# Kernel optimization log

Measured on AMD Instinct MI355X. Metric: run time of the kernel, lower is better.

Reference implementation:

```python
import jax, jax.numpy as jnp
import numpy as np

B, S, D, H = 2, 2048, 1024, 16
DK = D // H


def setup_inputs() -> dict:
    key = jax.random.key(0)
    ks = jax.random.split(key, 8)
    Q = jax.random.normal(ks[0], (B, S, D), dtype=jnp.float32)
    K = jax.random.normal(ks[1], (B, S, D), dtype=jnp.float32)
    V = jax.random.normal(ks[2], (B, S, D), dtype=jnp.float32)
    # causal mask (1 = keep), broadcastable to [B, H, S, S]
    mask = jnp.tril(jnp.ones((S, S), dtype=bool))[None, None, :, :]
    # xavier_uniform for [D, D]: bound = sqrt(6 / (D + D))
    bound = float(np.sqrt(6.0 / (D + D)))
    def xavier(k):
        return jax.random.uniform(k, (D, D), jnp.float32, -bound, bound)
    Wq, Wk, Wv, Wo = xavier(ks[3]), xavier(ks[4]), xavier(ks[5]), xavier(ks[6])
    bq = jnp.zeros((D,), jnp.float32)
    bk = jnp.zeros((D,), jnp.float32)
    bv = jnp.zeros((D,), jnp.float32)
    bo = jnp.zeros((D,), jnp.float32)
    return {"Q": Q, "K": K, "V": V, "mask": mask,
            "Wq": Wq, "bq": bq, "Wk": Wk, "bk": bk,
            "Wv": Wv, "bv": bv, "Wo": Wo, "bo": bo}


def _split_heads(x):
    # [B, S, D] -> [B, H, S, DK]
    b, s, _ = x.shape
    return x.reshape(b, s, H, DK).transpose(0, 2, 1, 3)


def reference(Q, K, V, mask, Wq, bq, Wk, bk, Wv, bv, Wo, bo):
    # linear projections (torch Linear: x @ W.T + b)
    q = _split_heads(Q @ Wq.T + bq)  # [B, H, S, DK]
    k = _split_heads(K @ Wk.T + bk)
    v = _split_heads(V @ Wv.T + bv)
    scale = 1.0 / jnp.sqrt(jnp.asarray(DK, q.dtype))
    scores = jnp.einsum('bhqd,bhkd->bhqk', q, k) * scale  # [B, H, S, S]
    scores = jnp.where(mask, scores, jnp.asarray(-1e9, scores.dtype))
    attn = jax.nn.softmax(scores, axis=-1)
    ctx = jnp.einsum('bhqk,bhkd->bhqd', attn, v)  # [B, H, S, DK]
    ctx = ctx.transpose(0, 2, 1, 3).reshape(Q.shape[0], Q.shape[1], D)
    out = ctx @ Wo.T + bo  # dropout is identity in eval mode
    return out, attn
```

## Files before the change

### kernel.cpp

```cpp
#include <hip/hip_runtime.h>
#include <hip/hip_bf16.h>

#define B_  2
#define S_  2048
#define D_  1024
#define H_  16
#define DK_ 64
#define M_  (B_*S_)
#define NT_ (S_/64)
#define NE_ (B_*S_*D_)
#define NW_ (D_*D_)

typedef __attribute__((ext_vector_type(8))) short short8;
typedef __attribute__((ext_vector_type(4))) float f32x4;

static __device__ __forceinline__ unsigned short f2bf(float f) {
    union { float f; unsigned u; } v; v.f = f;
    unsigned r = (v.u + 0x7fffu + ((v.u >> 16) & 1u)) >> 16;
    return (unsigned short)r;
}

static __device__ __forceinline__ void gload16(const void* g, void* l) {
    __builtin_amdgcn_global_load_lds((const __attribute__((address_space(1))) void*)g,
                                     (__attribute__((address_space(3))) void*)l, 16, 0, 0);
}

__global__ __launch_bounds__(256) void conv7(const float* __restrict__ q,  const float* __restrict__ k,
                                             const float* __restrict__ v,  const float* __restrict__ wq,
                                             const float* __restrict__ wk, const float* __restrict__ wv,
                                             const float* __restrict__ wo, unsigned short* __restrict__ ws)
{
    const float* src[7] = {q, k, v, wq, wk, wv, wo};
    const int    n4[7]  = {NE_/4, NE_/4, NE_/4, NW_/4, NW_/4, NW_/4, NW_/4};
    size_t off = 0;
    #pragma unroll
    for (int seg = 0; seg < 7; ++seg) {
        unsigned short* dst = ws + off;
        for (int i = blockIdx.x*256 + threadIdx.x; i < n4[seg]; i += gridDim.x*256) {
            float4 x = ((const float4*)src[seg])[i];
            union { unsigned short u[4]; unsigned long long ll; } cv;
            cv.u[0]=f2bf(x.x); cv.u[1]=f2bf(x.y); cv.u[2]=f2bf(x.z); cv.u[3]=f2bf(x.w);
            ((unsigned long long*)dst)[i] = cv.ll;
        }
        off += (size_t)n4[seg]*4;
    }
}

__global__ __launch_bounds__(256) void gemm_bt(const unsigned short* __restrict__ A0,
                                               const unsigned short* __restrict__ W0,
                                               const float* __restrict__ b0,
                                               const float* __restrict__ b1,
                                               const float* __restrict__ b2,
                                               void* __restrict__ outv,
                                               void* __restrict__ outv2,
                                               int out_mode)
{
    __shared__ unsigned short as_[128][64];
    __shared__ unsigned short bs_[128][64];

    const int tid  = threadIdx.x;
    const int wave = tid >> 6;
    const int lane = tid & 63;
    const int lq   = lane & 15, quad = lane >> 4;

    const int g     = blockIdx.x;
    const int xcd   = g & 7;
    const int local = g >> 3;
    const int m_loc = local & 3;
    const int rest  = local >> 2;
    const int n_t   = rest & 7;
    const int z     = rest >> 3;

    const int m0 = (xcd*4 + m_loc) * 128;
    const int n0 = n_t * 128;
    const int wm = (wave >> 1) * 64, wn = (wave & 1) * 64;

    const unsigned short* A  = A0 + (size_t)z * NE_;
    const unsigned short* Bt = W0 + (size_t)z * NW_;
    const float* bias = (z == 0) ? b0 : (z == 1 ? b1 : b2);

    f32x4 acc[4][4] = {};

    for (int k0 = 0; k0 < D_; k0 += 64) {
        __syncthreads();
        #pragma unroll
        for (int i = 0; i < 4; ++i) {
            const int p = tid + i*256, row = p >> 3, c = (p & 7) ^ (row & 7);
            gload16(A + (size_t)(m0+row)*D_ + k0 + c*8,
                    (char*)as_ + (size_t)(wave*64 + i*256)*16);
        }
        #pragma unroll
        for (int i = 0; i < 4; ++i) {
            const int p = tid + i*256, row = p >> 3, c = (p & 7) ^ (row & 7);
            gload16(Bt + (size_t)(n0+row)*D_ + k0 + c*8,
                    (char*)bs_ + (size_t)(wave*64 + i*256)*16);
        }
        __syncthreads();

        #pragma unroll
        for (int kk = 0; kk < 2; ++kk) {
            short8 a[4], b[4];
            #pragma unroll
            for (int i = 0; i < 4; ++i) {
                const int row = wm + i*16 + lq;
                a[i] = *(const short8*)((const char*)as_ + row*128 + (((kk*4+quad) ^ (row&7))*16));
            }
            #pragma unroll
            for (int j = 0; j < 4; ++j) {
                const int row = wn + j*16 + lq;
                b[j] = *(const short8*)((const char*)bs_ + row*128 + (((kk*4+quad) ^ (row&7))*16));
            }
            #pragma unroll
            for (int i = 0; i < 4; ++i)
                #pragma unroll
                for (int j = 0; j < 4; ++j)
                    acc[i][j] = __builtin_amdgcn_mfma_f32_16x16x32_bf16(a[i], b[j], acc[i][j], 0, 0, 0);
        }
    }

    float bcol[4];
    #pragma unroll
    for (int j = 0; j < 4; ++j) bcol[j] = bias[n0 + wn + j*16 + lq];

    if (out_mode == 0) {
        float* out = (float*)outv;
        #pragma unroll
        for (int i = 0; i < 4; ++i)
            #pragma unroll
            for (int j = 0; j < 4; ++j) {
                const int col = n0 + wn + j*16 + lq;
                #pragma unroll
                for (int r = 0; r < 4; ++r) {
                    const int m = m0 + wm + i*16 + quad*4 + r;
                    out[(size_t)m*D_ + col] = acc[i][j][r] + bcol[j];
                }
            }
    } else if (z < 2) {
        unsigned short* out = (unsigned short*)outv + (size_t)z * NE_;
        #pragma unroll
        for (int i = 0; i < 4; ++i)
            #pragma unroll
            for (int j = 0; j < 4; ++j) {
                const int col = n0 + wn + j*16 + lq;
                const int h = col >> 6, dk = col & 63;
                #pragma unroll
                for (int r = 0; r < 4; ++r) {
                    const int m  = m0 + wm + i*16 + quad*4 + r;
                    const int bb = m >> 11, s = m & (S_-1);
                    out[(((size_t)(bb*H_ + h))*S_ + s)*DK_ + dk] = f2bf(acc[i][j][r] + bcol[j]);
                }
            }
    } else {
        unsigned short* out = (unsigned short*)outv2;
        #pragma unroll
        for (int i = 0; i < 4; ++i)
            #pragma unroll
            for (int j = 0; j < 4; ++j) {
                const int col = n0 + wn + j*16 + lq;
                const int h = col >> 6, dk = col & 63;
                const int m  = m0 + wm + i*16 + quad*4;
                const int bb = m >> 11, s = m & (S_-1);
                union { unsigned short u[4]; unsigned long long ll; } pk;
                #pragma unroll
                for (int r = 0; r < 4; ++r) pk.u[r] = f2bf(acc[i][j][r] + bcol[j]);
                *(unsigned long long*)&out[(((size_t)(bb*H_ + h))*DK_ + dk)*S_ + s] = pk.ll;
            }
    }
}

__global__ __launch_bounds__(256) void attn_mfma(const unsigned short* __restrict__ q,
                                                 const unsigned short* __restrict__ k,
                                                 const unsigned short* __restrict__ vt,
                                                 float* __restrict__ attn,
                                                 unsigned short* __restrict__ ctx)
{
    __shared__ unsigned short qs[2][64][64];
    __shared__ unsigned short ks[64][64];
    __shared__ unsigned short vts[64][64];
    __shared__ unsigned short es[4][16][72];

    const int tid  = threadIdx.x;
    const int wave = tid >> 6, lane = tid & 63;
    const int lq   = lane & 15, quad = lane >> 4;

    const int g = blockIdx.x;
    const int xcd = g & 7, i5 = g >> 3;
    const int x = i5 >> 2;
    const int bhid = xcd + 8*(i5 & 3);
    const int h = bhid & (H_-1), b = bhid >> 4;

    const int itA = x, itB = NT_-1 - x;
    const size_t bh = (size_t)(b*H_ + h);
    const unsigned short* kb  = k  + bh*S_*DK_;
    const unsigned short* vtb = vt + bh*(size_t)DK_*S_;
    const unsigned short* qbA = q + (bh*S_ + (size_t)itA*64) * DK_;
    const unsigned short* qbB = q + (bh*S_ + (size_t)itB*64) * DK_;
    float* attn_bA = attn + bh*(size_t)S_*S_ + (size_t)itA*64*S_;
    float* attn_bB = attn + bh*(size_t)S_*S_ + (size_t)itB*64*S_;

    #pragma unroll
    for (int t = 0; t < 2; ++t) {
        const unsigned short* qb = t ? qbB : qbA;
        #pragma unroll
        for (int i = 0; i < 2; ++i) {
            const int p = tid + i*256, row = p >> 3, c = (p & 7) ^ (row & 7);
            gload16(qb + (size_t)row*DK_ + c*8,
                    (char*)&qs[t][0][0] + (size_t)(wave*64 + i*256)*16);
        }
    }
    __syncthreads();

    const int wr0  = wave*16;
    const int rgA0 = itA*64 + wr0 + quad*4;
    const int rgB0 = itB*64 + wr0 + quad*4;

    short8 aA0, aA1, aB0, aB1;
    {
        const int row = wr0 + lq;
        const int s0 = ((quad)     ^ (row & 7)) * 16;
        const int s1 = ((4 + quad) ^ (row & 7)) * 16;
        aA0 = *(const short8*)((const char*)&qs[0][row][0] + s0);
        aA1 = *(const short8*)((const char*)&qs[0][row][0] + s1);
        aB0 = *(const short8*)((const char*)&qs[1][row][0] + s0);
        aB1 = *(const short8*)((const char*)&qs[1][row][0] + s1);
    }

    float rsA[4] = {0.f,0.f,0.f,0.f}, rsB[4] = {0.f,0.f,0.f,0.f};
    for (int jt = 0; jt <= itB; ++jt) {
        __syncthreads();
        #pragma unroll
        for (int i = 0; i < 2; ++i) {
            const int p = tid + i*256, row = p >> 3, c = (p & 7) ^ (row & 7);
            gload16(kb + ((size_t)jt*64 + row)*DK_ + c*8,
                    (char*)&ks[0][0] + (size_t)(wave*64 + i*256)*16);
        }
        __syncthreads();
        const int actA = (jt <= itA);
        #pragma unroll
        for (int j = 0; j < 4; ++j) {
            const int krow = j*16 + lq;
            const int s0 = ((quad)     ^ (krow & 7)) * 16;
            const int s1 = ((4 + quad) ^ (krow & 7)) * 16;
            const short8 b0 = *(const short8*)((const char*)&ks[krow][0] + s0);
            const short8 b1 = *(const short8*)((const char*)&ks[krow][0] + s1);
            const int cg = jt*64 + j*16 + lq;
            {
                f32x4 s = {};
                s = __builtin_amdgcn_mfma_f32_16x16x32_bf16(aB0, b0, s, 0, 0, 0);
                s = __builtin_amdgcn_mfma_f32_16x16x32_bf16(aB1, b1, s, 0, 0, 0);
                #pragma unroll
                for (int r = 0; r < 4; ++r)
                    if (cg <= rgB0 + r) rsB[r] += __expf(s[r]*0.125f);
            }
            if (actA) {
                f32x4 s = {};
                s = __builtin_amdgcn_mfma_f32_16x16x32_bf16(aA0, b0, s, 0, 0, 0);
                s = __builtin_amdgcn_mfma_f32_16x16x32_bf16(aA1, b1, s, 0, 0, 0);
                #pragma unroll
                for (int r = 0; r < 4; ++r)
                    if (cg <= rgA0 + r) rsA[r] += __expf(s[r]*0.125f);
            }
        }
    }
    #pragma unroll
    for (int m = 1; m < 16; m <<= 1)
        #pragma unroll
        for (int r = 0; r < 4; ++r) {
            rsA[r] += __shfl_xor(rsA[r], m, 64);
            rsB[r] += __shfl_xor(rsB[r], m, 64);
        }
    float invA[4], invB[4];
    #pragma unroll
    for (int r = 0; r < 4; ++r) { invA[r] = 1.0f/rsA[r]; invB[r] = 1.0f/rsB[r]; }

    f32x4 cA[4] = {}, cB[4] = {};
    for (int jt = 0; jt <= itB; ++jt) {
        __syncthreads();
        #pragma unroll
        for (int i = 0; i < 2; ++i) {
            const int p = tid + i*256, row = p >> 3, c = (p & 7) ^ (row & 7);
            gload16(kb + ((size_t)jt*64 + row)*DK_ + c*8,
                    (char*)&ks[0][0] + (size_t)(wave*64 + i*256)*16);
            gload16(vtb + (size_t)row*S_ + jt*64 + c*8,
                    (char*)&vts[0][0] + (size_t)(wave*64 + i*256)*16);
        }
        __syncthreads();
        const int actA = (jt <= itA);

        #pragma unroll
        for (int j = 0; j < 4; ++j) {
            const int krow = j*16 + lq;
            const int s0 = ((quad)     ^ (krow & 7)) * 16;
            const int s1 = ((4 + quad) ^ (krow & 7)) * 16;
            const short8 b0 = *(const short8*)((const char*)&ks[krow][0] + s0);
            const short8 b1 = *(const short8*)((const char*)&ks[krow][0] + s1);
            const int cg = jt*64 + j*16 + lq;
            f32x4 s = {};
            s = __builtin_amdgcn_mfma_f32_16x16x32_bf16(aB0, b0, s, 0, 0, 0);
            s = __builtin_amdgcn_mfma_f32_16x16x32_bf16(aB1, b1, s, 0, 0, 0);
            #pragma unroll
            for (int r = 0; r < 4; ++r) {
                const float e = (cg <= rgB0 + r) ? __expf(s[r]*0.125f)*invB[r] : 0.f;
                attn_bB[(size_t)(wr0 + quad*4 + r)*S_ + cg] = e;
                es[wave][quad*4 + r][j*16 + lq] = f2bf(e);
            }
        }
        {
            const short8 p0 = *(const short8*)&es[wave][lq][quad*8];
            const short8 p1 = *(const short8*)&es[wave][lq][32 + quad*8];
            #pragma unroll
            for (int j = 0; j < 4; ++j) {
                const int vrow = j*16 + lq;
                const int s0 = ((quad)     ^ (vrow & 7)) * 16;
                const int s1 = ((4 + quad) ^ (vrow & 7)) * 16;
                cB[j] = __builtin_amdgcn_mfma_f32_16x16x32_bf16(
                    p0, *(const short8*)((const char*)&vts[vrow][0] + s0), cB[j], 0, 0, 0);
                cB[j] = __builtin_amdgcn_mfma_f32_16x16x32_bf16(
                    p1, *(const short8*)((const char*)&vts[vrow][0] + s1), cB[j], 0, 0, 0);
            }
        }

        if (actA) {
            #pragma unroll
            for (int j = 0; j < 4; ++j) {
                const int krow = j*16 + lq;
                const int s0 = ((quad)     ^ (krow & 7)) * 16;
                const int s1 = ((4 + quad) ^ (krow & 7)) * 16;
                const short8 b0 = *(const short8*)((const char*)&ks[krow][0] + s0);
                const short8 b1 = *(const short8*)((const char*)&ks[krow][0] + s1);
                const int cg = jt*64 + j*16 + lq;
                f32x4 s = {};
                s = __builtin_amdgcn_mfma_f32_16x16x32_bf16(aA0, b0, s, 0, 0, 0);
                s = __builtin_amdgcn_mfma_f32_16x16x32_bf16(aA1, b1, s, 0, 0, 0);
                #pragma unroll
                for (int r = 0; r < 4; ++r) {
                    const float e = (cg <= rgA0 + r) ? __expf(s[r]*0.125f)*invA[r] : 0.f;
                    attn_bA[(size_t)(wr0 + quad*4 + r)*S_ + cg] = e;
                    es[wave][quad*4 + r][j*16 + lq] = f2bf(e);
                }
            }
            const short8 p0 = *(const short8*)&es[wave][lq][quad*8];
            const short8 p1 = *(const short8*)&es[wave][lq][32 + quad*8];
            #pragma unroll
            for (int j = 0; j < 4; ++j) {
                const int vrow = j*16 + lq;
                const int s0 = ((quad)     ^ (vrow & 7)) * 16;
                const int s1 = ((4 + quad) ^ (vrow & 7)) * 16;
                cA[j] = __builtin_amdgcn_mfma_f32_16x16x32_bf16(
                    p0, *(const short8*)((const char*)&vts[vrow][0] + s0), cA[j], 0, 0, 0);
                cA[j] = __builtin_amdgcn_mfma_f32_16x16x32_bf16(
                    p1, *(const short8*)((const char*)&vts[vrow][0] + s1), cA[j], 0, 0, 0);
            }
        }
    }

    #pragma unroll
    for (int j = 0; j < 4; ++j) {
        const int dk = j*16 + lq;
        #pragma unroll
        for (int r = 0; r < 4; ++r) {
            const int sA = itA*64 + wr0 + quad*4 + r;
            const int sB = itB*64 + wr0 + quad*4 + r;
            ctx[((size_t)b*S_ + sA)*D_ + h*DK_ + dk] = f2bf(cA[j][r]);
            ctx[((size_t)b*S_ + sB)*D_ + h*DK_ + dk] = f2bf(cB[j][r]);
        }
    }

    const float4 z4 = make_float4(0.f, 0.f, 0.f, 0.f);
    {
        const int zc0 = (itA+1)*64;
        float* rowp = attn_bA + (size_t)(tid >> 2)*S_;
        for (int c = zc0 + (tid & 3)*4; c < S_; c += 16) *(float4*)&rowp[c] = z4;
    }
    {
        const int zc0 = (itB+1)*64;
        if (zc0 < S_) {
            float* rowp = attn_bB + (size_t)(tid >> 2)*S_;
            for (int c = zc0 + (tid & 3)*4; c < S_; c += 16) *(float4*)&rowp[c] = z4;
        }
    }
}

extern "C" void kernel_launch(void* const* d_in, const int* in_sizes, int n_in,
                              void* d_out, int out_size, void* d_ws, size_t ws_size,
                              hipStream_t stream)
{
    const float* Q  = (const float*)d_in[0];
    const float* K  = (const float*)d_in[1];
    const float* V  = (const float*)d_in[2];
    const float* Wq = (const float*)d_in[4];
    const float* bq = (const float*)d_in[5];
    const float* Wk = (const float*)d_in[6];
    const float* bk = (const float*)d_in[7];
    const float* Wv = (const float*)d_in[8];
    const float* bv = (const float*)d_in[9];
    const float* Wo = (const float*)d_in[10];
    const float* bo = (const float*)d_in[11];

    float* out  = (float*)d_out;
    float* attn = out + (size_t)B_*S_*D_;

    unsigned short* ws = (unsigned short*)d_ws;
    const size_t R  = (size_t)NE_;
    const size_t W1 = (size_t)NW_;
    unsigned short* Qb  = ws;
    unsigned short* Wqb = ws + 3*R;
    unsigned short* Wob = Wqb + 3*W1;
    unsigned short* qp  = Wob + W1;
    unsigned short* kp  = qp + R;
    unsigned short* vtw = qp + 2*R;
    unsigned short* ctx = vtw + R;

    conv7<<<2048, 256, 0, stream>>>(Q, K, V, Wq, Wk, Wv, Wo, ws);

    gemm_bt<<<768, 256, 0, stream>>>(Qb, Wqb, bq, bk, bv, qp, vtw, 1);
    attn_mfma<<<(NT_/2)*H_*B_, 256, 0, stream>>>(qp, kp, vtw, attn, ctx);
    gemm_bt<<<256, 256, 0, stream>>>(ctx, Wob, bo, bo, bo, out, nullptr, 0);
}
```

Before: 804.2 us.

## Single-pass unnormalized softmax with bf16 scratch and separate normalization kernel

Removes the first pass over K that computed row sums. Each score block is now exponentiated once, unnormalized, with the log2(e)/sqrt(dk) scale folded into the Q projection and a raw v_exp_f32. Unnormalized probabilities go to a bf16 scratch buffer, and the context is scaled by the inverse row sum at the end. A new kernel reads the scratch plus per-row inverse sums and writes the fp32 attention matrix, including the zeroed upper triangle. There is no running max subtraction, so this relies on scores staying small enough not to overflow exp. It also adds an extra bf16 write and read of the full S×S matrix, and the stored attention is rounded through bf16.

```diff
diff --git a/kernel.cpp b/kernel.cpp
--- a/kernel.cpp
+++ b/kernel.cpp
@@ -14,10 +14,20 @@
 typedef __attribute__((ext_vector_type(8))) short short8;
 typedef __attribute__((ext_vector_type(4))) float f32x4;
 
+#define QSCALE 0.18033688011112042f
+
 static __device__ __forceinline__ unsigned short f2bf(float f) {
     union { float f; unsigned u; } v; v.f = f;
     unsigned r = (v.u + 0x7fffu + ((v.u >> 16) & 1u)) >> 16;
     return (unsigned short)r;
+}
+static __device__ __forceinline__ float bf2f(unsigned short u) {
+    union { unsigned u; float f; } v; v.u = (unsigned)u << 16; return v.f;
+}
+static __device__ __forceinline__ float exp2v(float x) {
+    float r;
+    asm("v_exp_f32 %0, %1" : "=v"(r) : "v"(x));
+    return r;
 }
 
 static __device__ __forceinline__ void gload16(const void* g, void* l) {
@@ -136,6 +146,7 @@
                 }
             }
     } else if (z < 2) {
+        const float sc = (z == 0) ? QSCALE : 1.0f;
         unsigned short* out = (unsigned short*)outv + (size_t)z * NE_;
         #pragma unroll
         for (int i = 0; i < 4; ++i)
@@ -147,7 +158,7 @@
                 for (int r = 0; r < 4; ++r) {
                     const int m  = m0 + wm + i*16 + quad*4 + r;
                     const int bb = m >> 11, s = m & (S_-1);
-                    out[(((size_t)(bb*H_ + h))*S_ + s)*DK_ + dk] = f2bf(acc[i][j][r] + bcol[j]);
+                    out[(((size_t)(bb*H_ + h))*S_ + s)*DK_ + dk] = f2bf((acc[i][j][r] + bcol[j]) * sc);
                 }
             }
     } else {
@@ -171,7 +182,8 @@
 __global__ __launch_bounds__(256) void attn_mfma(const unsigned short* __restrict__ q,
                                                  const unsigned short* __restrict__ k,
                                                  const unsigned short* __restrict__ vt,
-                                                 float* __restrict__ attn,
+                                                 unsigned short* __restrict__ eb,
+                                                 float* __restrict__ invb,
                                                  unsigned short* __restrict__ ctx)
 {
     __shared__ unsigned short qs[2][64][64];
@@ -195,8 +207,8 @@
     const unsigned short* vtb = vt + bh*(size_t)DK_*S_;
     const unsigned short* qbA = q + (bh*S_ + (size_t)itA*64) * DK_;
     const unsigned short* qbB = q + (bh*S_ + (size_t)itB*64) * DK_;
-    float* attn_bA = attn + bh*(size_t)S_*S_ + (size_t)itA*64*S_;
-    float* attn_bB = attn + bh*(size_t)S_*S_ + (size_t)itB*64*S_;
+    unsigned short* ebA = eb + (bh*S_ + (size_t)itA*64 + wave*16)*S_;
+    unsigned short* ebB = eb + (bh*S_ + (size_t)itB*64 + wave*16)*S_;
 
     #pragma unroll
     for (int t = 0; t < 2; ++t) {
@@ -226,54 +238,8 @@
     }
 
     float rsA[4] = {0.f,0.f,0.f,0.f}, rsB[4] = {0.f,0.f,0.f,0.f};
-    for (int jt = 0; jt <= itB; ++jt) {
-        __syncthreads();
-        #pragma unroll
-        for (int i = 0; i < 2; ++i) {
-            const int p = tid + i*256, row = p >> 3, c = (p & 7) ^ (row & 7);
-            gload16(kb + ((size_t)jt*64 + row)*DK_ + c*8,
-                    (char*)&ks[0][0] + (size_t)(wave*64 + i*256)*16);
-        }
-        __syncthreads();
-        const int actA = (jt <= itA);
-        #pragma unroll
-        for (int j = 0; j < 4; ++j) {
-            const int krow = j*16 + lq;
-            const int s0 = ((quad)     ^ (krow & 7)) * 16;
-            const int s1 = ((4 + quad) ^ (krow & 7)) * 16;
-            const short8 b0 = *(const short8*)((const char*)&ks[krow][0] + s0);
-            const short8 b1 = *(const short8*)((const char*)&ks[krow][0] + s1);
-            const int cg = jt*64 + j*16 + lq;
-            {
-                f32x4 s = {};
-                s = __builtin_amdgcn_mfma_f32_16x16x32_bf16(aB0, b0, s, 0, 0, 0);
-                s = __builtin_amdgcn_mfma_f32_16x16x32_bf16(aB1, b1, s, 0, 0, 0);
-                #pragma unroll
-                for (int r = 0; r < 4; ++r)
-                    if (cg <= rgB0 + r) rsB[r] += __expf(s[r]*0.125f);
-            }
-            if (actA) {
-                f32x4 s = {};
-                s = __builtin_amdgcn_mfma_f32_16x16x32_bf16(aA0, b0, s, 0, 0, 0);
-                s = __builtin_amdgcn_mfma_f32_16x16x32_bf16(aA1, b1, s, 0, 0, 0);
-                #pragma unroll
-                for (int r = 0; r < 4; ++r)
-                    if (cg <= rgA0 + r) rsA[r] += __expf(s[r]*0.125f);
-            }
-        }
-    }
-    #pragma unroll
-    for (int m = 1; m < 16; m <<= 1)
-        #pragma unroll
-        for (int r = 0; r < 4; ++r) {
-            rsA[r] += __shfl_xor(rsA[r], m, 64);
-            rsB[r] += __shfl_xor(rsB[r], m, 64);
-        }
-    float invA[4], invB[4];
-    #pragma unroll
-    for (int r = 0; r < 4; ++r) { invA[r] = 1.0f/rsA[r]; invB[r] = 1.0f/rsB[r]; }
-
     f32x4 cA[4] = {}, cB[4] = {};
+
     for (int jt = 0; jt <= itB; ++jt) {
         __syncthreads();
         #pragma unroll
@@ -287,25 +253,48 @@
         __syncthreads();
         const int actA = (jt <= itA);
 
-        #pragma unroll
-        for (int j = 0; j < 4; ++j) {
-            const int krow = j*16 + lq;
-            const int s0 = ((quad)     ^ (krow & 7)) * 16;
-            const int s1 = ((4 + quad) ^ (krow & 7)) * 16;
-            const short8 b0 = *(const short8*)((const char*)&ks[krow][0] + s0);
-            const short8 b1 = *(const short8*)((const char*)&ks[krow][0] + s1);
-            const int cg = jt*64 + j*16 + lq;
-            f32x4 s = {};
-            s = __builtin_amdgcn_mfma_f32_16x16x32_bf16(aB0, b0, s, 0, 0, 0);
-            s = __builtin_amdgcn_mfma_f32_16x16x32_bf16(aB1, b1, s, 0, 0, 0);
-            #pragma unroll
-            for (int r = 0; r < 4; ++r) {
-                const float e = (cg <= rgB0 + r) ? __expf(s[r]*0.125f)*invB[r] : 0.f;
-                attn_bB[(size_t)(wr0 + quad*4 + r)*S_ + cg] = e;
-                es[wave][quad*4 + r][j*16 + lq] = f2bf(e);
-            }
-        }
         {
+            f32x4 sa[4];
+            #pragma unroll
+            for (int j = 0; j < 4; ++j) {
+                const int krow = j*16 + lq;
+                const int s0 = ((quad)     ^ (krow & 7)) * 16;
+                const int s1 = ((4 + quad) ^ (krow & 7)) * 16;
+                f32x4 s = {};
+                s = __builtin_amdgcn_mfma_f32_16x16x32_bf16(
+                    aB0, *(const short8*)((const char*)&ks[krow][0] + s0), s, 0, 0, 0);
+                s = __builtin_amdgcn_mfma_f32_16x16x32_bf16(
+                    aB1, *(const short8*)((const char*)&ks[krow][0] + s1), s, 0, 0, 0);
+                sa[j] = s;
+            }
+            if (jt == itB) {
+                #pragma unroll
+                for (int j = 0; j < 4; ++j) {
+                    const int cg = jt*64 + j*16 + lq;
+                    #pragma unroll
+                    for (int r = 0; r < 4; ++r) {
+                        float e = exp2v(sa[j][r]);
+                        if (cg > rgB0 + r) e = 0.f;
+                        rsB[r] += e;
+                        es[wave][quad*4 + r][j*16 + lq] = f2bf(e);
+                    }
+                }
+            } else {
+                #pragma unroll
+                for (int j = 0; j < 4; ++j)
+                    #pragma unroll
+                    for (int r = 0; r < 4; ++r) {
+                        const float e = exp2v(sa[j][r]);
+                        rsB[r] += e;
+                        es[wave][quad*4 + r][j*16 + lq] = f2bf(e);
+                    }
+            }
+            #pragma unroll
+            for (int i = 0; i < 2; ++i) {
+                const int ch = lane + i*64, r16 = ch >> 3, c8 = ch & 7;
+                *(short8*)(ebB + (size_t)r16*S_ + jt*64 + c8*8) =
+                    *(const short8*)&es[wave][r16][c8*8];
+            }
             const short8 p0 = *(const short8*)&es[wave][lq][quad*8];
             const short8 p1 = *(const short8*)&es[wave][lq][32 + quad*8];
             #pragma unroll
@@ -321,23 +310,46 @@
         }
 
         if (actA) {
+            f32x4 sa[4];
             #pragma unroll
             for (int j = 0; j < 4; ++j) {
                 const int krow = j*16 + lq;
                 const int s0 = ((quad)     ^ (krow & 7)) * 16;
                 const int s1 = ((4 + quad) ^ (krow & 7)) * 16;
-                const short8 b0 = *(const short8*)((const char*)&ks[krow][0] + s0);
-                const short8 b1 = *(const short8*)((const char*)&ks[krow][0] + s1);
-                const int cg = jt*64 + j*16 + lq;
                 f32x4 s = {};
-                s = __builtin_amdgcn_mfma_f32_16x16x32_bf16(aA0, b0, s, 0, 0, 0);
-                s = __builtin_amdgcn_mfma_f32_16x16x32_bf16(aA1, b1, s, 0, 0, 0);
-                #pragma unroll
-                for (int r = 0; r < 4; ++r) {
-                    const float e = (cg <= rgA0 + r) ? __expf(s[r]*0.125f)*invA[r] : 0.f;
-                    attn_bA[(size_t)(wr0 + quad*4 + r)*S_ + cg] = e;
-                    es[wave][quad*4 + r][j*16 + lq] = f2bf(e);
+                s = __builtin_amdgcn_mfma_f32_16x16x32_bf16(
+                    aA0, *(const short8*)((const char*)&ks[krow][0] + s0), s, 0, 0, 0);
+                s = __builtin_amdgcn_mfma_f32_16x16x32_bf16(
+                    aA1, *(const short8*)((const char*)&ks[krow][0] + s1), s, 0, 0, 0);
+                sa[j] = s;
+            }
+            if (jt == itA) {
+                #pragma unroll
+                for (int j = 0; j < 4; ++j) {
+                    const int cg = jt*64 + j*16 + lq;
+                    #pragma unroll
+                    for (int r = 0; r < 4; ++r) {
+                        float e = exp2v(sa[j][r]);
+                        if (cg > rgA0 + r) e = 0.f;
+                        rsA[r] += e;
+                        es[wave][quad*4 + r][j*16 + lq] = f2bf(e);
+                    }
                 }
+            } else {
+                #pragma unroll
+                for (int j = 0; j < 4; ++j)
+                    #pragma unroll
+                    for (int r = 0; r < 4; ++r) {
+                        const float e = exp2v(sa[j][r]);
+                        rsA[r] += e;
+                        es[wave][quad*4 + r][j*16 + lq] = f2bf(e);
+                    }
+            }
+            #pragma unroll
+            for (int i = 0; i < 2; ++i) {
+                const int ch = lane + i*64, r16 = ch >> 3, c8 = ch & 7;
+                *(short8*)(ebA + (size_t)r16*S_ + jt*64 + c8*8) =
+                    *(const short8*)&es[wave][r16][c8*8];
             }
             const short8 p0 = *(const short8*)&es[wave][lq][quad*8];
             const short8 p1 = *(const short8*)&es[wave][lq][32 + quad*8];
@@ -355,28 +367,65 @@
     }
 
     #pragma unroll
+    for (int m = 1; m < 16; m <<= 1)
+        #pragma unroll
+        for (int r = 0; r < 4; ++r) {
+            rsA[r] += __shfl_xor(rsA[r], m, 64);
+            rsB[r] += __shfl_xor(rsB[r], m, 64);
+        }
+    float invA[4], invB[4];
+    #pragma unroll
+    for (int r = 0; r < 4; ++r) { invA[r] = 1.0f/rsA[r]; invB[r] = 1.0f/rsB[r]; }
+
+    if (lq == 0) {
+        #pragma unroll
+        for (int r = 0; r < 4; ++r) {
+            invb[bh*S_ + itA*64 + wr0 + quad*4 + r] = invA[r];
+            invb[bh*S_ + itB*64 + wr0 + quad*4 + r] = invB[r];
+        }
+    }
+
+    #pragma unroll
     for (int j = 0; j < 4; ++j) {
         const int dk = j*16 + lq;
         #pragma unroll
         for (int r = 0; r < 4; ++r) {
             const int sA = itA*64 + wr0 + quad*4 + r;
             const int sB = itB*64 + wr0 + quad*4 + r;
-            ctx[((size_t)b*S_ + sA)*D_ + h*DK_ + dk] = f2bf(cA[j][r]);
-            ctx[((size_t)b*S_ + sB)*D_ + h*DK_ + dk] = f2bf(cB[j][r]);
-        }
-    }
-
+            ctx[((size_t)b*S_ + sA)*D_ + h*DK_ + dk] = f2bf(cA[j][r]*invA[r]);
+            ctx[((size_t)b*S_ + sB)*D_ + h*DK_ + dk] = f2bf(cB[j][r]*invB[r]);
+        }
+    }
+}
+
+__global__ __launch_bounds__(256) void norm_attn(const unsigned short* __restrict__ eb,
+                                                 const float* __restrict__ invb,
+                                                 float* __restrict__ attn)
+{
+    const int tid = threadIdx.x;
+    const int grp = blockIdx.x;
+    const int bh  = grp >> 7;
+    const int r0  = (grp & 127) << 4;
+    const size_t base = (size_t)bh * S_ * S_;
     const float4 z4 = make_float4(0.f, 0.f, 0.f, 0.f);
-    {
-        const int zc0 = (itA+1)*64;
-        float* rowp = attn_bA + (size_t)(tid >> 2)*S_;
-        for (int c = zc0 + (tid & 3)*4; c < S_; c += 16) *(float4*)&rowp[c] = z4;
-    }
-    {
-        const int zc0 = (itB+1)*64;
-        if (zc0 < S_) {
-            float* rowp = attn_bB + (size_t)(tid >> 2)*S_;
-            for (int c = zc0 + (tid & 3)*4; c < S_; c += 16) *(float4*)&rowp[c] = z4;
+
+    #pragma unroll 4
+    for (int r = 0; r < 16; ++r) {
+        const int rg = r0 + r;
+        const int limit = ((rg >> 6) + 1) << 6;
+        float* dst = attn + base + (size_t)rg*S_ + tid*8;
+        if (tid*8 < limit) {
+            const float iv = invb[bh*S_ + rg];
+            union { short8 v; unsigned short u[8]; } pk;
+            pk.v = *(const short8*)(eb + base + (size_t)rg*S_ + tid*8);
+            float4 o0, o1;
+            o0.x = bf2f(pk.u[0])*iv; o0.y = bf2f(pk.u[1])*iv;
+            o0.z = bf2f(pk.u[2])*iv; o0.w = bf2f(pk.u[3])*iv;
+            o1.x = bf2f(pk.u[4])*iv; o1.y = bf2f(pk.u[5])*iv;
+            o1.z = bf2f(pk.u[6])*iv; o1.w = bf2f(pk.u[7])*iv;
+            *(float4*)dst = o0; *(float4*)(dst + 4) = o1;
+        } else {
+            *(float4*)dst = z4; *(float4*)(dst + 4) = z4;
         }
     }
 }
@@ -410,10 +459,13 @@
     unsigned short* kp  = qp + R;
     unsigned short* vtw = qp + 2*R;
     unsigned short* ctx = vtw + R;
+    unsigned short* eb  = ctx + R;
+    float*          invb = (float*)(eb + (size_t)B_*H_*S_*S_);
 
     conv7<<<2048, 256, 0, stream>>>(Q, K, V, Wq, Wk, Wv, Wo, ws);
 
     gemm_bt<<<768, 256, 0, stream>>>(Qb, Wqb, bq, bk, bv, qp, vtw, 1);
-    attn_mfma<<<(NT_/2)*H_*B_, 256, 0, stream>>>(qp, kp, vtw, attn, ctx);
+    attn_mfma<<<(NT_/2)*H_*B_, 256, 0, stream>>>(qp, kp, vtw, eb, invb, ctx);
+    norm_attn<<<B_*H_*S_/16, 256, 0, stream>>>(eb, invb, attn);
     gemm_bt<<<256, 256, 0, stream>>>(ctx, Wob, bo, bo, bo, out, nullptr, 0);
 }
```

Result: slower. 824.4 us (+2.5%).
